# Kernel optimization log

Measured on AMD Instinct MI355X. Metric: run time of the kernel, lower is better.

## Reference

```python
import jax, jax.numpy as jnp
import numpy as np

HEADS = 8
DIM_HEAD = 64
SCALE = DIM_HEAD ** -0.5


def setup_inputs() -> dict:
    key = jax.random.key(0)
    k1, k2, k3, k4 = jax.random.split(key, 4)
    b, n, dim = 4, 1024, 512
    inner = HEADS * DIM_HEAD  # 512
    x = jax.random.normal(k1, (b, n, dim), dtype=jnp.float32)
    spd = jax.random.normal(k2, (b, HEADS, n, n), dtype=jnp.float32)
    head_keep = jnp.ones((HEADS,), dtype=jnp.float32)  # deterministic stand-in for binomial head drop
    w_qkv = jax.random.normal(k3, (dim, 3 * inner), dtype=jnp.float32) * (dim ** -0.5)
    w_out = jax.random.normal(k4, (inner, dim), dtype=jnp.float32) * (inner ** -0.5)
    b_out = jnp.zeros((dim,), dtype=jnp.float32)
    return {"x": x, "spd": spd, "head_keep": head_keep, "w_qkv": w_qkv, "w_out": w_out, "b_out": b_out}


def reference(x, spd, head_keep, w_qkv, w_out, b_out):
    b, n, dim = x.shape
    qkv = x @ w_qkv  # [b, n, 3*inner]
    q, k, v = jnp.split(qkv, 3, axis=-1)

    def to_heads(t):  # [b, n, h*d] -> [b, h, n, d]
        return t.reshape(b, n, HEADS, DIM_HEAD).transpose(0, 2, 1, 3)

    q, k, v = to_heads(q), to_heads(k), to_heads(v)
    dots = jnp.einsum('bhid,bhjd->bhij', q, k) * SCALE + spd  # [b, h, n, n]
    attn = jax.nn.softmax(dots, axis=-1)
    # random head drop + rescale: attn * mask * H / sum(keep)
    keep_sum = jnp.sum(head_keep)
    attn = attn * (head_keep[None, :, None, None] * (HEADS / keep_sum))
    out = jnp.einsum('bhij,bhjd->bhid', attn, v)  # [b, h, n, d]
    out = out.transpose(0, 2, 1, 3).reshape(b, n, HEADS * DIM_HEAD)
    return out @ w_out + b_out
```

## Files before the change

### kernel.cpp

```cpp
#include <hip/hip_runtime.h>
#include <math.h>

#define NSEQ   1024
#define HEADS  8
#define DHEAD  64
#define SCALE  0.125f
#define LOG2E  1.4426950408889634f

typedef unsigned int u32;
typedef unsigned short u16;
typedef short short8 __attribute__((ext_vector_type(8)));
typedef __bf16 bf16x2 __attribute__((ext_vector_type(2)));
typedef __bf16 bf16x8 __attribute__((ext_vector_type(8)));
typedef float f32x4  __attribute__((ext_vector_type(4)));
typedef float f32x16 __attribute__((ext_vector_type(16)));

__device__ __forceinline__ u16 f2bf(float f) {
    __bf16 h = (__bf16)f;
    return __builtin_bit_cast(u16, h);
}
__device__ __forceinline__ u32 pk2(float lo, float hi) {
    bf16x2 v; v[0] = (__bf16)lo; v[1] = (__bf16)hi;
    return __builtin_bit_cast(u32, v);
}
__device__ __forceinline__ float exp2_fast(float x) {
#if __has_builtin(__builtin_amdgcn_exp2f)
    return __builtin_amdgcn_exp2f(x);
#else
    return exp2f(x);
#endif
}
__device__ __forceinline__ f32x4 mfma16(short8 a, short8 b, f32x4 c) {
    return __builtin_amdgcn_mfma_f32_16x16x32_bf16(a, b, c, 0, 0, 0);
}
__device__ __forceinline__ f32x16 mfma32(short8 a, short8 b, f32x16 c) {
    return __builtin_amdgcn_mfma_f32_32x32x16_bf16(a, b, c, 0, 0, 0);
}

__global__ __launch_bounds__(256) void prep(const float* __restrict__ x,
                                            const float* __restrict__ wqkv,
                                            const float* __restrict__ wout,
                                            u16* __restrict__ x_bf,
                                            u16* __restrict__ wqkvT,
                                            u16* __restrict__ woutT) {
    __shared__ float T[64][65];
    const int t = threadIdx.x;
    const int bb = blockIdx.x;
    if (bb < 1024) {
        int i = (bb * 256 + t) * 8;
        float4 a = *(const float4*)&x[i];
        float4 b = *(const float4*)&x[i + 4];
        bf16x8 v;
        v[0] = (__bf16)a.x; v[1] = (__bf16)a.y; v[2] = (__bf16)a.z; v[3] = (__bf16)a.w;
        v[4] = (__bf16)b.x; v[5] = (__bf16)b.y; v[6] = (__bf16)b.z; v[7] = (__bf16)b.w;
        *(short8*)&x_bf[i] = __builtin_bit_cast(short8, v);
        return;
    }
    const float* in; u16* outp; int K, N, n0, k0;
    if (bb < 1216) {
        int bid = bb - 1024;
        in = wqkv; outp = wqkvT; K = 512; N = 1536;
        n0 = (bid % 24) * 64; k0 = (bid / 24) * 64;
    } else {
        int bid = bb - 1216;
        in = wout; outp = woutT; K = 512; N = 512;
        n0 = (bid % 8) * 64; k0 = (bid / 8) * 64;
    }
    #pragma unroll
    for (int rep = 0; rep < 4; ++rep) {
        int r = rep * 16 + (t >> 4), c = (t & 15) * 4;
        float4 v = *(const float4*)&in[(size_t)(k0 + r) * N + n0 + c];
        T[r][c + 0] = v.x; T[r][c + 1] = v.y; T[r][c + 2] = v.z; T[r][c + 3] = v.w;
    }
    __syncthreads();
    const int nl = t >> 2, kb = (t & 3) * 16;
    bf16x8 s0, s1;
    #pragma unroll
    for (int e = 0; e < 8; ++e) s0[e] = (__bf16)T[kb + e][nl];
    #pragma unroll
    for (int e = 0; e < 8; ++e) s1[e] = (__bf16)T[kb + 8 + e][nl];
    *(short8*)&outp[(size_t)(n0 + nl) * K + k0 + kb]     = __builtin_bit_cast(short8, s0);
    *(short8*)&outp[(size_t)(n0 + nl) * K + k0 + kb + 8] = __builtin_bit_cast(short8, s1);
}

__global__ __launch_bounds__(256) void gemm_qkv_mfma(const u16* __restrict__ xb,
                                                     const u16* __restrict__ wT,
                                                     u16* __restrict__ qb,
                                                     u16* __restrict__ kb,
                                                     u16* __restrict__ vT) {
    __shared__ u16 As[128][72];
    __shared__ u16 Bs[64][72];
    const int t = threadIdx.x, lane = t & 63, w = t >> 6;
    const int wm = w >> 1, wn = w & 1;
    const int l15 = lane & 15, l4 = lane >> 4;
    const int bid = blockIdx.x;
    const int swz = (bid & 7) * 96 + (bid >> 3);
    const int j0 = (swz % 24) * 64, i0 = (swz / 24) * 128;
    const int which = j0 / 512;
    const int b = i0 >> 10;

    f32x4 acc[8];
    #pragma unroll
    for (int i = 0; i < 8; ++i) acc[i] = (f32x4){0.f, 0.f, 0.f, 0.f};

    const int arow0 = t >> 2, c16 = (t & 3) * 16;

    short8 ra[4], rb2[2];
    #pragma unroll
    for (int rep = 0; rep < 2; ++rep)
        #pragma unroll
        for (int q = 0; q < 2; ++q)
            ra[rep * 2 + q] = *(const short8*)&xb[(size_t)(i0 + rep * 64 + arow0) * 512 + c16 + q * 8];
    #pragma unroll
    for (int q = 0; q < 2; ++q)
        rb2[q] = *(const short8*)&wT[(size_t)(j0 + arow0) * 512 + c16 + q * 8];

    for (int kt = 0; kt < 8; ++kt) {
        __syncthreads();
        #pragma unroll
        for (int rep = 0; rep < 2; ++rep)
            #pragma unroll
            for (int q = 0; q < 2; ++q)
                *(short8*)&As[rep * 64 + arow0][c16 + q * 8] = ra[rep * 2 + q];
        #pragma unroll
        for (int q = 0; q < 2; ++q)
            *(short8*)&Bs[arow0][c16 + q * 8] = rb2[q];
        __syncthreads();
        if (kt < 7) {
            int k0 = (kt + 1) * 64;
            #pragma unroll
            for (int rep = 0; rep < 2; ++rep)
                #pragma unroll
                for (int q = 0; q < 2; ++q)
                    ra[rep * 2 + q] = *(const short8*)&xb[(size_t)(i0 + rep * 64 + arow0) * 512 + k0 + c16 + q * 8];
            #pragma unroll
            for (int q = 0; q < 2; ++q)
                rb2[q] = *(const short8*)&wT[(size_t)(j0 + arow0) * 512 + k0 + c16 + q * 8];
        }
        #pragma unroll
        for (int ks = 0; ks < 2; ++ks) {
            if (which < 2) {
                short8 af[4], bf[2];
                #pragma unroll
                for (int m = 0; m < 4; ++m)
                    af[m] = *(const short8*)&As[wm * 64 + m * 16 + l15][ks * 32 + l4 * 8];
                #pragma unroll
                for (int n = 0; n < 2; ++n)
                    bf[n] = *(const short8*)&Bs[wn * 32 + n * 16 + l15][ks * 32 + l4 * 8];
                #pragma unroll
                for (int m = 0; m < 4; ++m)
                    #pragma unroll
                    for (int n = 0; n < 2; ++n)
                        acc[m * 2 + n] = mfma16(af[m], bf[n], acc[m * 2 + n]);
            } else {
                short8 af[2], bf[4];
                #pragma unroll
                for (int mj = 0; mj < 2; ++mj)
                    af[mj] = *(const short8*)&Bs[wn * 32 + mj * 16 + l15][ks * 32 + l4 * 8];
                #pragma unroll
                for (int ni = 0; ni < 4; ++ni)
                    bf[ni] = *(const short8*)&As[wm * 64 + ni * 16 + l15][ks * 32 + l4 * 8];
                #pragma unroll
                for (int mj = 0; mj < 2; ++mj)
                    #pragma unroll
                    for (int ni = 0; ni < 4; ++ni)
                        acc[mj * 4 + ni] = mfma16(af[mj], bf[ni], acc[mj * 4 + ni]);
            }
        }
    }

    if (which < 2) {
        u16* dst = (which == 0) ? qb : kb;
        const int h = (j0 & 511) >> 6;
        #pragma unroll
        for (int m = 0; m < 4; ++m)
            #pragma unroll
            for (int n = 0; n < 2; ++n) {
                int d = wn * 32 + n * 16 + l15;
                #pragma unroll
                for (int r = 0; r < 4; ++r) {
                    int tok = i0 + wm * 64 + m * 16 + l4 * 4 + r;
                    dst[(((size_t)(b * HEADS + h)) * NSEQ + (tok & 1023)) * DHEAD + d] =
                        f2bf(acc[m * 2 + n][r]);
                }
            }
    } else {
        const int h = (j0 - 1024) >> 6;
        #pragma unroll
        for (int mj = 0; mj < 2; ++mj)
            #pragma unroll
            for (int ni = 0; ni < 4; ++ni) {
                int tok = i0 + wm * 64 + ni * 16 + l15;
                #pragma unroll
                for (int r = 0; r < 4; ++r) {
                    int d = wn * 32 + mj * 16 + l4 * 4 + r;
                    vT[(((size_t)(b * HEADS + h)) * DHEAD + d) * NSEQ + (tok & 1023)] =
                        f2bf(acc[mj * 4 + ni][r]);
                }
            }
    }
}

__global__ __launch_bounds__(256) void attn_mfma(const u16* __restrict__ qb,
                                                 const u16* __restrict__ kb,
                                                 const u16* __restrict__ vT,
                                                 const float* __restrict__ spd,
                                                 const float* __restrict__ head_keep,
                                                 u16* __restrict__ ab) {
    __shared__ u16 Qs[128][72];
    __shared__ u16 Kd[2][64][72];
    __shared__ u16 Vd[2][64][72];
    __shared__ float Sd[2][128][65];

    const int t = threadIdx.x, lane = t & 63, w = t >> 6;
    const int hi = lane >> 5, li = lane & 31;
    const int bid = blockIdx.x;
    const int swz = (bid & 7) * 32 + (bid >> 3);
    const int bh = swz >> 3, it = swz & 7;
    const int b = bh >> 3, h = bh & 7;
    const int i0 = it * 128;

    const u16* qh = qb + (size_t)bh * NSEQ * DHEAD;
    const u16* kh = kb + (size_t)bh * NSEQ * DHEAD;
    const u16* vh = vT + (size_t)bh * DHEAD * NSEQ;
    const float* sp = spd + (size_t)bh * NSEQ * NSEQ;

    #pragma unroll
    for (int rep = 0; rep < 4; ++rep) {
        int row = rep * 32 + (t >> 3), c8 = (t & 7) * 8;
        *(short8*)&Qs[row][c8] = *(const short8*)&qh[(size_t)(i0 + row) * DHEAD + c8];
    }

    const int krow = t >> 3, kc8 = (t & 7) * 8;
    const int srow = t >> 4, sc = (t & 15) * 4;

    short8 rk[2], rv[2];
    float4 rs[8];
    #pragma unroll
    for (int rep = 0; rep < 2; ++rep) {
        rk[rep] = *(const short8*)&kh[(size_t)(rep * 32 + krow) * DHEAD + kc8];
        rv[rep] = *(const short8*)&vh[(size_t)(rep * 32 + krow) * NSEQ + kc8];
    }
    #pragma unroll
    for (int rep = 0; rep < 8; ++rep)
        rs[rep] = *(const float4*)&sp[(size_t)(i0 + rep * 16 + srow) * NSEQ + sc];
    #pragma unroll
    for (int rep = 0; rep < 2; ++rep) {
        *(short8*)&Kd[0][rep * 32 + krow][kc8] = rk[rep];
        *(short8*)&Vd[0][rep * 32 + krow][kc8] = rv[rep];
    }
    #pragma unroll
    for (int rep = 0; rep < 8; ++rep) {
        int rrow = rep * 16 + srow;
        Sd[0][rrow][sc + 0] = rs[rep].x * LOG2E;
        Sd[0][rrow][sc + 1] = rs[rep].y * LOG2E;
        Sd[0][rrow][sc + 2] = rs[rep].z * LOG2E;
        Sd[0][rrow][sc + 3] = rs[rep].w * LOG2E;
    }
    #pragma unroll
    for (int rep = 0; rep < 2; ++rep) {
        rk[rep] = *(const short8*)&kh[(size_t)(64 + rep * 32 + krow) * DHEAD + kc8];
        rv[rep] = *(const short8*)&vh[(size_t)(rep * 32 + krow) * NSEQ + 64 + kc8];
    }
    #pragma unroll
    for (int rep = 0; rep < 8; ++rep)
        rs[rep] = *(const float4*)&sp[(size_t)(i0 + rep * 16 + srow) * NSEQ + 64 + sc];
    __syncthreads();

    float m_s = -1e30f, l_s = 0.f;
    f32x16 o0 = {}, o1 = {};
    #pragma unroll
    for (int r = 0; r < 16; ++r) { o0[r] = 0.f; o1[r] = 0.f; }

    for (int jt = 0; jt < 16; ++jt) {
        const int cur = jt & 1;

        f32x16 s2[2];
        #pragma unroll
        for (int kg = 0; kg < 2; ++kg) {
            #pragma unroll
            for (int r = 0; r < 16; ++r) s2[kg][r] = 0.f;
            #pragma unroll
            for (int ds = 0; ds < 4; ++ds) {
                short8 ak = *(const short8*)&Kd[cur][kg * 32 + li][ds * 16 + hi * 8];
                short8 bq = *(const short8*)&Qs[w * 32 + li][ds * 16 + hi * 8];
                s2[kg] = mfma32(ak, bq, s2[kg]);
            }
        }

        float p2[32];
        #pragma unroll
        for (int kg = 0; kg < 2; ++kg)
            #pragma unroll
            for (int r = 0; r < 16; ++r) {
                int key = kg * 32 + (r & 3) + 8 * (r >> 2) + 4 * hi;
                p2[kg * 16 + r] = fmaf(s2[kg][r], SCALE * LOG2E, Sd[cur][w * 32 + li][key]);
            }
        float m16[16];
        #pragma unroll
        for (int r = 0; r < 16; ++r) m16[r] = fmaxf(p2[r], p2[r + 16]);
        float m8v[8];
        #pragma unroll
        for (int r = 0; r < 8; ++r) m8v[r] = fmaxf(m16[r], m16[r + 8]);
        float m4v[4];
        #pragma unroll
        for (int r = 0; r < 4; ++r) m4v[r] = fmaxf(m8v[r], m8v[r + 4]);
        float pmax = fmaxf(fmaxf(m4v[0], m4v[1]), fmaxf(m4v[2], m4v[3]));
        pmax = fmaxf(pmax, __shfl_xor(pmax, 32));

        if (!__all(pmax <= m_s + 12.0f)) {
            float mnew = fmaxf(m_s, pmax);
            float fac = exp2_fast(m_s - mnew);
            m_s = mnew;
            l_s *= fac;
            #pragma unroll
            for (int r = 0; r < 16; ++r) {
                int ip = (r & 3) + 8 * (r >> 2) + 4 * hi;
                float fr = __shfl(fac, ip);
                o0[r] *= fr; o1[r] *= fr;
            }
        }

        float p[32];
        float sa0 = 0.f, sa1 = 0.f, sa2 = 0.f, sa3 = 0.f;
        #pragma unroll
        for (int r = 0; r < 32; r += 4) {
            p[r + 0] = exp2_fast(p2[r + 0] - m_s); sa0 += p[r + 0];
            p[r + 1] = exp2_fast(p2[r + 1] - m_s); sa1 += p[r + 1];
            p[r + 2] = exp2_fast(p2[r + 2] - m_s); sa2 += p[r + 2];
            p[r + 3] = exp2_fast(p2[r + 3] - m_s); sa3 += p[r + 3];
        }
        float rsum = (sa0 + sa1) + (sa2 + sa3);
        rsum += __shfl_xor(rsum, 32);
        l_s += rsum;

        short8 pf[4];
        #pragma unroll
        for (int ks = 0; ks < 4; ++ks) {
            int rb = (ks >> 1) * 16 + (ks & 1) * 8;
            u32 a0 = pk2(p[rb + 0], p[rb + 1]);
            u32 a1 = pk2(p[rb + 2], p[rb + 3]);
            u32 a2 = pk2(p[rb + 4], p[rb + 5]);
            u32 a3 = pk2(p[rb + 6], p[rb + 7]);
            u32 x0 = (u32)__shfl_xor((int)a0, 32);
            u32 x1 = (u32)__shfl_xor((int)a1, 32);
            u32 x2 = (u32)__shfl_xor((int)a2, 32);
            u32 x3 = (u32)__shfl_xor((int)a3, 32);
            union { u32 u[4]; short8 v; } c4;
            c4.u[0] = hi ? x2 : a0;
            c4.u[1] = hi ? x3 : a1;
            c4.u[2] = hi ? a2 : x0;
            c4.u[3] = hi ? a3 : x1;
            pf[ks] = c4.v;
        }

        #pragma unroll
        for (int ks = 0; ks < 4; ++ks) {
            short8 v0f = *(const short8*)&Vd[cur][li][ks * 16 + hi * 8];
            short8 v1f = *(const short8*)&Vd[cur][32 + li][ks * 16 + hi * 8];
            o0 = mfma32(pf[ks], v0f, o0);
            o1 = mfma32(pf[ks], v1f, o1);
        }

        if (jt < 15) {
            const int nxt = cur ^ 1;
            #pragma unroll
            for (int rep = 0; rep < 2; ++rep) {
                *(short8*)&Kd[nxt][rep * 32 + krow][kc8] = rk[rep];
                *(short8*)&Vd[nxt][rep * 32 + krow][kc8] = rv[rep];
            }
            #pragma unroll
            for (int rep = 0; rep < 8; ++rep) {
                int rrow = rep * 16 + srow;
                Sd[nxt][rrow][sc + 0] = rs[rep].x * LOG2E;
                Sd[nxt][rrow][sc + 1] = rs[rep].y * LOG2E;
                Sd[nxt][rrow][sc + 2] = rs[rep].z * LOG2E;
                Sd[nxt][rrow][sc + 3] = rs[rep].w * LOG2E;
            }
            if (jt < 14) {
                int j0n = (jt + 2) * 64;
                #pragma unroll
                for (int rep = 0; rep < 2; ++rep) {
                    rk[rep] = *(const short8*)&kh[(size_t)(j0n + rep * 32 + krow) * DHEAD + kc8];
                    rv[rep] = *(const short8*)&vh[(size_t)(rep * 32 + krow) * NSEQ + j0n + kc8];
                }
                #pragma unroll
                for (int rep = 0; rep < 8; ++rep)
                    rs[rep] = *(const float4*)&sp[(size_t)(i0 + rep * 16 + srow) * NSEQ + j0n + sc];
            }
            __syncthreads();
        }
    }

    float ksum = 0.f;
    #pragma unroll
    for (int i = 0; i < HEADS; ++i) ksum += head_keep[i];
    const float hscale = head_keep[h] * (float)HEADS / ksum;
    const float inv = hscale / l_s;
    #pragma unroll
    for (int r = 0; r < 16; ++r) {
        int ip = (r & 3) + 8 * (r >> 2) + 4 * hi;
        float invr = __shfl(inv, ip);
        int tok = i0 + w * 32 + ip;
        size_t base = ((size_t)(b * NSEQ) + tok) * 512 + h * DHEAD;
        ab[base + li]      = f2bf(o0[r] * invr);
        ab[base + 32 + li] = f2bf(o1[r] * invr);
    }
}

__global__ __launch_bounds__(256) void gemm_out_mfma(const u16* __restrict__ abuf,
                                                     const u16* __restrict__ wT,
                                                     const float* __restrict__ bias,
                                                     float* __restrict__ out) {
    __shared__ u16 As[64][72];
    __shared__ u16 Bs[64][72];
    const int t = threadIdx.x, lane = t & 63, w = t >> 6;
    const int wm = w >> 1, wn = w & 1;
    const int l15 = lane & 15, l4 = lane >> 4;
    const int bid = blockIdx.x;
    const int swz = (bid & 7) * 64 + (bid >> 3);
    const int j0 = (swz % 8) * 64, i0 = (swz / 8) * 64;

    f32x4 acc[2][2];
    #pragma unroll
    for (int m = 0; m < 2; ++m)
        #pragma unroll
        for (int n = 0; n < 2; ++n) acc[m][n] = (f32x4){0.f, 0.f, 0.f, 0.f};

    const int row0 = t >> 2, c16 = (t & 3) * 16;
    short8 rav[2], rbv[2];
    #pragma unroll
    for (int q = 0; q < 2; ++q) {
        rav[q] = *(const short8*)&abuf[(size_t)(i0 + row0) * 512 + c16 + q * 8];
        rbv[q] = *(const short8*)&wT[(size_t)(j0 + row0) * 512 + c16 + q * 8];
    }

    for (int kt = 0; kt < 8; ++kt) {
        __syncthreads();
        #pragma unroll
        for (int q = 0; q < 2; ++q) {
            *(short8*)&As[row0][c16 + q * 8] = rav[q];
            *(short8*)&Bs[row0][c16 + q * 8] = rbv[q];
        }
        __syncthreads();
        if (kt < 7) {
            int k0 = (kt + 1) * 64;
            #pragma unroll
            for (int q = 0; q < 2; ++q) {
                rav[q] = *(const short8*)&abuf[(size_t)(i0 + row0) * 512 + k0 + c16 + q * 8];
                rbv[q] = *(const short8*)&wT[(size_t)(j0 + row0) * 512 + k0 + c16 + q * 8];
            }
        }
        #pragma unroll
        for (int ks = 0; ks < 2; ++ks) {
            short8 af[2], bf[2];
            #pragma unroll
            for (int m = 0; m < 2; ++m)
                af[m] = *(const short8*)&As[wm * 32 + m * 16 + l15][ks * 32 + l4 * 8];
            #pragma unroll
            for (int n = 0; n < 2; ++n)
                bf[n] = *(const short8*)&Bs[wn * 32 + n * 16 + l15][ks * 32 + l4 * 8];
            #pragma unroll
            for (int m = 0; m < 2; ++m)
                #pragma unroll
                for (int n = 0; n < 2; ++n)
                    acc[m][n] = mfma16(af[m], bf[n], acc[m][n]);
        }
    }

    #pragma unroll
    for (int m = 0; m < 2; ++m)
        #pragma unroll
        for (int n = 0; n < 2; ++n) {
            int col = j0 + wn * 32 + n * 16 + l15;
            float bb = bias[col];
            #pragma unroll
            for (int r = 0; r < 4; ++r) {
                int row = i0 + wm * 32 + m * 16 + l4 * 4 + r;
                out[(size_t)row * 512 + col] = acc[m][n][r] + bb;
            }
        }
}

extern "C" void kernel_launch(void* const* d_in, const int* in_sizes, int n_in,
                              void* d_out, int out_size, void* d_ws, size_t ws_size,
                              hipStream_t stream) {
    const float* x         = (const float*)d_in[0];
    const float* spd       = (const float*)d_in[1];
    const float* head_keep = (const float*)d_in[2];
    const float* w_qkv     = (const float*)d_in[3];
    const float* w_out     = (const float*)d_in[4];
    const float* b_out     = (const float*)d_in[5];
    float* out = (float*)d_out;

    char* ws = (char*)d_ws;
    u16* x_bf   = (u16*)(ws);
    u16* wqkvT  = (u16*)(ws + (4u << 20));
    u16* woutT  = (u16*)(ws + (4u << 20) + 1572864);
    u16* qb     = (u16*)(ws + (6u << 20));
    u16* kb     = (u16*)(ws + (10u << 20));
    u16* vT     = (u16*)(ws + (14u << 20));
    u16* ab     = (u16*)(ws + (18u << 20));

    prep<<<1280, 256, 0, stream>>>(x, w_qkv, w_out, x_bf, wqkvT, woutT);
    gemm_qkv_mfma<<<768, 256, 0, stream>>>(x_bf, wqkvT, qb, kb, vT);
    attn_mfma<<<256, 256, 0, stream>>>(qb, kb, vT, spd, head_keep, ab);
    gemm_out_mfma<<<512, 256, 0, stream>>>(ab, woutT, b_out, out);
}
```

Measured before the change: 62.70 us.

## Store spd bias as bf16 in LDS, keep Q in registers, target two blocks/CU

The attention kernel now keeps its Q fragments in registers instead of a shared Qs tile, and stores the staged spd bias in LDS as bf16 rather than fp32. Together these cut shared memory per block from roughly 102KB to roughly 52KB. Launch bounds request two blocks per CU so more waves can hide latency. The bf16 bias loses precision in the softmax logits, and the occupancy hint may force register spills.

```diff
diff --git a/kernel.cpp b/kernel.cpp
--- a/kernel.cpp
+++ b/kernel.cpp
@@ -22,6 +22,10 @@
 __device__ __forceinline__ u32 pk2(float lo, float hi) {
     bf16x2 v; v[0] = (__bf16)lo; v[1] = (__bf16)hi;
     return __builtin_bit_cast(u32, v);
+}
+__device__ __forceinline__ float bf2f(u16 b) {
+    u32 u = ((u32)b) << 16;
+    return __builtin_bit_cast(float, u);
 }
 __device__ __forceinline__ float exp2_fast(float x) {
 #if __has_builtin(__builtin_amdgcn_exp2f)
@@ -201,16 +205,15 @@
     }
 }
 
-__global__ __launch_bounds__(256) void attn_mfma(const u16* __restrict__ qb,
-                                                 const u16* __restrict__ kb,
-                                                 const u16* __restrict__ vT,
-                                                 const float* __restrict__ spd,
-                                                 const float* __restrict__ head_keep,
-                                                 u16* __restrict__ ab) {
-    __shared__ u16 Qs[128][72];
+__global__ __launch_bounds__(256, 2) void attn_mfma(const u16* __restrict__ qb,
+                                                    const u16* __restrict__ kb,
+                                                    const u16* __restrict__ vT,
+                                                    const float* __restrict__ spd,
+                                                    const float* __restrict__ head_keep,
+                                                    u16* __restrict__ ab) {
     __shared__ u16 Kd[2][64][72];
     __shared__ u16 Vd[2][64][72];
-    __shared__ float Sd[2][128][65];
+    __shared__ u16 Sd[2][128][66];
 
     const int t = threadIdx.x, lane = t & 63, w = t >> 6;
     const int hi = lane >> 5, li = lane & 31;
@@ -225,11 +228,10 @@
     const u16* vh = vT + (size_t)bh * DHEAD * NSEQ;
     const float* sp = spd + (size_t)bh * NSEQ * NSEQ;
 
-    #pragma unroll
-    for (int rep = 0; rep < 4; ++rep) {
-        int row = rep * 32 + (t >> 3), c8 = (t & 7) * 8;
-        *(short8*)&Qs[row][c8] = *(const short8*)&qh[(size_t)(i0 + row) * DHEAD + c8];
-    }
+    short8 qreg[4];
+    #pragma unroll
+    for (int ds = 0; ds < 4; ++ds)
+        qreg[ds] = *(const short8*)&qh[(size_t)(i0 + w * 32 + li) * DHEAD + ds * 16 + hi * 8];
 
     const int krow = t >> 3, kc8 = (t & 7) * 8;
     const int srow = t >> 4, sc = (t & 15) * 4;
@@ -252,10 +254,8 @@
     #pragma unroll
     for (int rep = 0; rep < 8; ++rep) {
         int rrow = rep * 16 + srow;
-        Sd[0][rrow][sc + 0] = rs[rep].x * LOG2E;
-        Sd[0][rrow][sc + 1] = rs[rep].y * LOG2E;
-        Sd[0][rrow][sc + 2] = rs[rep].z * LOG2E;
-        Sd[0][rrow][sc + 3] = rs[rep].w * LOG2E;
+        *(u32*)&Sd[0][rrow][sc]     = pk2(rs[rep].x * LOG2E, rs[rep].y * LOG2E);
+        *(u32*)&Sd[0][rrow][sc + 2] = pk2(rs[rep].z * LOG2E, rs[rep].w * LOG2E);
     }
     #pragma unroll
     for (int rep = 0; rep < 2; ++rep) {
@@ -283,8 +283,7 @@
             #pragma unroll
             for (int ds = 0; ds < 4; ++ds) {
                 short8 ak = *(const short8*)&Kd[cur][kg * 32 + li][ds * 16 + hi * 8];
-                short8 bq = *(const short8*)&Qs[w * 32 + li][ds * 16 + hi * 8];
-                s2[kg] = mfma32(ak, bq, s2[kg]);
+                s2[kg] = mfma32(ak, qreg[ds], s2[kg]);
             }
         }
 
@@ -294,7 +293,8 @@
             #pragma unroll
             for (int r = 0; r < 16; ++r) {
                 int key = kg * 32 + (r & 3) + 8 * (r >> 2) + 4 * hi;
-                p2[kg * 16 + r] = fmaf(s2[kg][r], SCALE * LOG2E, Sd[cur][w * 32 + li][key]);
+                p2[kg * 16 + r] = fmaf(s2[kg][r], SCALE * LOG2E,
+                                       bf2f(Sd[cur][w * 32 + li][key]));
             }
         float m16[16];
         #pragma unroll
@@ -321,14 +321,13 @@
             }
         }
 
-        float p[32];
         float sa0 = 0.f, sa1 = 0.f, sa2 = 0.f, sa3 = 0.f;
         #pragma unroll
         for (int r = 0; r < 32; r += 4) {
-            p[r + 0] = exp2_fast(p2[r + 0] - m_s); sa0 += p[r + 0];
-            p[r + 1] = exp2_fast(p2[r + 1] - m_s); sa1 += p[r + 1];
-            p[r + 2] = exp2_fast(p2[r + 2] - m_s); sa2 += p[r + 2];
-            p[r + 3] = exp2_fast(p2[r + 3] - m_s); sa3 += p[r + 3];
+            p2[r + 0] = exp2_fast(p2[r + 0] - m_s); sa0 += p2[r + 0];
+            p2[r + 1] = exp2_fast(p2[r + 1] - m_s); sa1 += p2[r + 1];
+            p2[r + 2] = exp2_fast(p2[r + 2] - m_s); sa2 += p2[r + 2];
+            p2[r + 3] = exp2_fast(p2[r + 3] - m_s); sa3 += p2[r + 3];
         }
         float rsum = (sa0 + sa1) + (sa2 + sa3);
         rsum += __shfl_xor(rsum, 32);
@@ -338,10 +337,10 @@
         #pragma unroll
         for (int ks = 0; ks < 4; ++ks) {
             int rb = (ks >> 1) * 16 + (ks & 1) * 8;
-            u32 a0 = pk2(p[rb + 0], p[rb + 1]);
-            u32 a1 = pk2(p[rb + 2], p[rb + 3]);
-            u32 a2 = pk2(p[rb + 4], p[rb + 5]);
-            u32 a3 = pk2(p[rb + 6], p[rb + 7]);
+            u32 a0 = pk2(p2[rb + 0], p2[rb + 1]);
+            u32 a1 = pk2(p2[rb + 2], p2[rb + 3]);
+            u32 a2 = pk2(p2[rb + 4], p2[rb + 5]);
+            u32 a3 = pk2(p2[rb + 6], p2[rb + 7]);
             u32 x0 = (u32)__shfl_xor((int)a0, 32);
             u32 x1 = (u32)__shfl_xor((int)a1, 32);
             u32 x2 = (u32)__shfl_xor((int)a2, 32);
@@ -372,10 +371,8 @@
             #pragma unroll
             for (int rep = 0; rep < 8; ++rep) {
                 int rrow = rep * 16 + srow;
-                Sd[nxt][rrow][sc + 0] = rs[rep].x * LOG2E;
-                Sd[nxt][rrow][sc + 1] = rs[rep].y * LOG2E;
-                Sd[nxt][rrow][sc + 2] = rs[rep].z * LOG2E;
-                Sd[nxt][rrow][sc + 3] = rs[rep].w * LOG2E;
+                *(u32*)&Sd[nxt][rrow][sc]     = pk2(rs[rep].x * LOG2E, rs[rep].y * LOG2E);
+                *(u32*)&Sd[nxt][rrow][sc + 2] = pk2(rs[rep].z * LOG2E, rs[rep].w * LOG2E);
             }
             if (jt < 14) {
                 int j0n = (jt + 2) * 64;
```

Result: no change. 61.68 us (median of 2 runs) (-1.6%).
